# Performance work log

Hardware: AMD Instinct MI355X
Metric: run time of the kernel (lower is better)

Reference implementation:

```python
import jax, jax.numpy as jnp
import numpy as np

N_NODES = 4096
N_EDGES = 65536
BS = 16
LEAKY_SLOPE = 0.01
BN_EPS = 1e-5


def _init(key, shape, scale=0.02):
    return (jax.random.normal(key, shape, dtype=jnp.float32) * scale)


def setup_inputs() -> dict:
    key = jax.random.key(0)
    ks = jax.random.split(key, 20)
    x_in = jax.random.normal(ks[0], (N_NODES, 8500), dtype=jnp.float32)
    edge_index = jax.random.randint(ks[1], (2, N_EDGES), 0, N_NODES, dtype=jnp.int64)
    return {
        "x_in": x_in,
        "edge_index": edge_index,
        # SAGEConv params: Wl (neighbor lin, with bias), Wr (root lin, no bias)
        "W1l": _init(ks[2], (320, 8500)), "b1": jnp.zeros((320,), jnp.float32), "W1r": _init(ks[3], (320, 8500)),
        "W2l": _init(ks[4], (180, 320)),  "b2": jnp.zeros((180,), jnp.float32), "W2r": _init(ks[5], (180, 320)),
        "W3l": _init(ks[6], (90, 180)),   "b3": jnp.zeros((90,), jnp.float32),  "W3r": _init(ks[7], (90, 180)),
        "W4l": _init(ks[8], (50, 90)),    "b4": jnp.zeros((50,), jnp.float32),  "W4r": _init(ks[9], (50, 90)),
        "Wf1": _init(ks[10], (32, 50)),   "bf1": jnp.zeros((32,), jnp.float32),
        "Wf2": _init(ks[11], (16, 32)),   "bf2": jnp.zeros((16,), jnp.float32),
        "Wf3": _init(ks[12], (1, 16)),    "bf3": jnp.zeros((1,), jnp.float32),
    }


def _sage(x, src, dst, Wl, bl, Wr):
    # PyG SAGEConv: out = lin_l(mean_{j in N(i)} x_j) + lin_r(x_i)
    agg = jax.ops.segment_sum(x[src], dst, num_segments=N_NODES)          # [N, F]
    deg = jax.ops.segment_sum(jnp.ones_like(dst, dtype=x.dtype), dst, num_segments=N_NODES)
    mean = agg / jnp.maximum(deg, 1.0)[:, None]
    return mean @ Wl.T + bl + x @ Wr.T


def _leaky(x):
    return jnp.where(x >= 0, x, LEAKY_SLOPE * x)


def _bn(x):
    # F.batch_norm(x, None, None, training=True): per-feature, biased var, no affine
    m = jnp.mean(x, axis=0)
    v = jnp.mean((x - m) ** 2, axis=0)
    return (x - m) / jnp.sqrt(v + BN_EPS)


def reference(x_in, edge_index,
              W1l, b1, W1r, W2l, b2, W2r, W3l, b3, W3r, W4l, b4, W4r,
              Wf1, bf1, Wf2, bf2, Wf3, bf3):
    src, dst = edge_index[0], edge_index[1]
    x = _bn(_leaky(_sage(x_in, src, dst, W1l, b1, W1r)))
    x = _bn(_leaky(_sage(x, src, dst, W2l, b2, W2r)))
    x = _bn(_leaky(_sage(x, src, dst, W3l, b3, W3r)))
    x = _bn(_leaky(_sage(x, src, dst, W4l, b4, W4r)))
    # get_batch: label i -> floor(i / (N/BS)); global_add_pool == segment sum
    x = x.reshape(BS, N_NODES // BS, -1).sum(axis=1)                      # [BS, 50]
    x = x @ Wf1.T + bf1
    x = x @ Wf2.T + bf2
    x = x @ Wf3.T + bf3
    return x
```

## Files before the change

kernel.cpp:

```cpp
#include <hip/hip_runtime.h>
#include <stdint.h>

#define NN 4096
#define NE 65536
#define LEAKY 0.01f
#define BN_EPS 1e-5f

typedef float f32x4 __attribute__((ext_vector_type(4)));
typedef __bf16 bf16x8 __attribute__((ext_vector_type(8)));
typedef unsigned short u16x8 __attribute__((ext_vector_type(8)));

static __device__ __forceinline__ unsigned short f2bf(float v) {
  unsigned int u = __float_as_uint(v);
  u += 0x7fff + ((u >> 16) & 1);
  return (unsigned short)(u >> 16);
}

typedef __attribute__((address_space(1))) void gvoid;
typedef __attribute__((address_space(3))) void lvoid;

static __device__ __forceinline__ void async16(const void* g, void* l) {
  __builtin_amdgcn_global_load_lds((gvoid*)(uintptr_t)g,
                                   (lvoid*)(uint32_t)(uintptr_t)l, 16, 0, 0);
}


static __device__ __forceinline__ void pack_w_seg(int lblk, const float* __restrict__ Wl,
                                                  const float* __restrict__ Wr,
                                                  unsigned short* __restrict__ dst,
                                                  int Fout, int Fin, int Kp, int Np) {
  int nb = Kp >> 3;
  int idx = lblk * 256 + threadIdx.x;
  if (idx >= Np * nb) return;
  int row = idx / nb, kb = idx - row * nb;
  int g = kb >> 3, b = kb & 7;
  int dkb = (g << 3) | ((b + row) & 7);
  const float* src = nullptr;
  if (row < Fout)          src = Wl + (size_t)row * Fin;
  else if (row < 2 * Fout) src = Wr + (size_t)(row - Fout) * Fin;
  u16x8 st;
#pragma unroll
  for (int o = 0; o < 8; ++o) {
    int k = kb * 8 + o;
    float v = (src && k < Fin) ? src[k] : 0.f;
    st[o] = f2bf(v);
  }
  *(u16x8*)&dst[(size_t)row * Kp + dkb * 8] = st;
}

#define PX_BLK   17024
#define PW1_BLK   2660
#define PW2_BLK     60
#define PW3_BLK     24
#define PW4_BLK      8
#define CD_BLK     256
#define SETUP_BLK (PX_BLK + PW1_BLK + PW2_BLK + PW3_BLK + PW4_BLK + CD_BLK)

__global__ __launch_bounds__(256) void setup_all(
    const float* __restrict__ x, const int* __restrict__ dsti,
    const float* __restrict__ W1l, const float* __restrict__ W1r,
    const float* __restrict__ W2l, const float* __restrict__ W2r,
    const float* __restrict__ W3l, const float* __restrict__ W3r,
    const float* __restrict__ W4l, const float* __restrict__ W4r,
    unsigned short* __restrict__ xbf, unsigned short* __restrict__ wb1,
    unsigned short* __restrict__ wb2, unsigned short* __restrict__ wb3,
    unsigned short* __restrict__ wb4, int* __restrict__ deg) {
  int blk = blockIdx.x;
  if (blk < PX_BLK) {
    int idx = blk * 256 + threadIdx.x;
    int row = idx / 1064, kb = idx - row * 1064;
    int g = kb >> 3, b = kb & 7;
    int dkb = (g << 3) | ((b + row) & 7);
    const float* src = x + (size_t)row * 8500 + kb * 8;
    float v[8];
    if (kb < 1062) {
      f32x4 a = *(const f32x4*)src;
      f32x4 c = *(const f32x4*)(src + 4);
#pragma unroll
      for (int o = 0; o < 4; ++o) { v[o] = a[o]; v[o + 4] = c[o]; }
    } else {
#pragma unroll
      for (int o = 0; o < 8; ++o) {
        int k = kb * 8 + o;
        v[o] = (k < 8500) ? x[(size_t)row * 8500 + k] : 0.f;
      }
    }
    u16x8 st;
#pragma unroll
    for (int o = 0; o < 8; ++o) st[o] = f2bf(v[o]);
    *(u16x8*)&xbf[(size_t)row * 8512 + dkb * 8] = st;
  } else if (blk < PX_BLK + PW1_BLK) {
    pack_w_seg(blk - PX_BLK, W1l, W1r, wb1, 320, 8500, 8512, 640);
  } else if (blk < PX_BLK + PW1_BLK + PW2_BLK) {
    pack_w_seg(blk - PX_BLK - PW1_BLK, W2l, W2r, wb2, 180, 320, 320, 384);
  } else if (blk < PX_BLK + PW1_BLK + PW2_BLK + PW3_BLK) {
    pack_w_seg(blk - PX_BLK - PW1_BLK - PW2_BLK, W3l, W3r, wb3, 90, 180, 192, 256);
  } else if (blk < PX_BLK + PW1_BLK + PW2_BLK + PW3_BLK + PW4_BLK) {
    pack_w_seg(blk - PX_BLK - PW1_BLK - PW2_BLK - PW3_BLK, W4l, W4r, wb4, 50, 90, 128, 128);
  } else {
    int e = (blk - (SETUP_BLK - CD_BLK)) * 256 + threadIdx.x;
    atomicAdd(&deg[dsti[e]], 1);
  }
}


__global__ __launch_bounds__(1024) void scan_deg(const int* __restrict__ deg,
                                                 int* __restrict__ off) {
  __shared__ int s[NN];
  int t = threadIdx.x;
  for (int i = t; i < NN; i += 1024) s[i] = deg[i];
  __syncthreads();
  for (int step = 1; step < NN; step <<= 1) {
    int v[4];
#pragma unroll
    for (int j = 0; j < 4; ++j) {
      int i = t + j * 1024;
      v[j] = (i >= step) ? s[i - step] : 0;
    }
    __syncthreads();
#pragma unroll
    for (int j = 0; j < 4; ++j) s[t + j * 1024] += v[j];
    __syncthreads();
  }
  for (int i = t; i < NN; i += 1024) off[i] = (i == 0) ? 0 : s[i - 1];
}

__global__ void scatter_edges(const int* __restrict__ src_idx,
                              const int* __restrict__ dst_idx,
                              const int* __restrict__ off, int* __restrict__ cursor,
                              int* __restrict__ eix) {
  int e = blockIdx.x * 256 + threadIdx.x;
  if (e < NE) {
    int d = dst_idx[e];
    int pos = atomicAdd(&cursor[d], 1);
    eix[off[d] + pos] = src_idx[e];
  }
}

__global__ __launch_bounds__(256) void gemm_bt(const unsigned short* __restrict__ A,
                                               const unsigned short* __restrict__ B,
                                               float* __restrict__ C, int N, int K) {
  __shared__ unsigned short smem[2 * 128 * 64];
  unsigned short* As = smem;
  unsigned short* Bs = smem + 128 * 64;

  const int t = threadIdx.x;
  const int bm = blockIdx.x, bn = blockIdx.y;
  const int lane = t & 63;
  const int wave = t >> 6;
  const int wm = (wave & 1) * 64, wn = (wave >> 1) * 64;
  const int l16 = lane & 15, quad = lane >> 4;

  const int ksteps = K >> 6;
  const int gz = (int)gridDim.z;
  const int per = (ksteps + gz - 1) / gz;
  const int k0 = (int)blockIdx.z * per;
  int k1 = k0 + per; if (k1 > ksteps) k1 = ksteps;

  f32x4 zero = {0.f, 0.f, 0.f, 0.f};
  f32x4 acc[4][4];
#pragma unroll
  for (int i = 0; i < 4; ++i)
#pragma unroll
    for (int j = 0; j < 4; ++j) acc[i][j] = zero;

  const int srow = t >> 3;
  const int scol = (t & 7) * 8;
  const unsigned short* Abase = A + (size_t)(bm * 128) * K + scol;
  const unsigned short* Bbase = B + (size_t)(bn * 128) * K + scol;

  for (int kt = k0; kt < k1; ++kt) {
    const unsigned short* Ag = Abase + kt * 64;
    const unsigned short* Bg = Bbase + kt * 64;
#pragma unroll
    for (int p = 0; p < 4; ++p) {
      int row = p * 32 + srow;
      async16(Ag + (size_t)row * K, &As[row * 64 + scol]);
    }
#pragma unroll
    for (int p = 0; p < 4; ++p) {
      int row = p * 32 + srow;
      async16(Bg + (size_t)row * K, &Bs[row * 64 + scol]);
    }
    __syncthreads();
#pragma unroll
    for (int kh = 0; kh < 2; ++kh) {
      const int s8 = ((kh * 4 + quad + l16) & 7) * 8;
      bf16x8 af[4], bfr[4];
#pragma unroll
      for (int i = 0; i < 4; ++i)
        af[i] = *(const bf16x8*)&As[(wm + i * 16 + l16) * 64 + s8];
#pragma unroll
      for (int j = 0; j < 4; ++j)
        bfr[j] = *(const bf16x8*)&Bs[(wn + j * 16 + l16) * 64 + s8];
#pragma unroll
      for (int i = 0; i < 4; ++i)
#pragma unroll
        for (int j = 0; j < 4; ++j)
          acc[i][j] = __builtin_amdgcn_mfma_f32_16x16x32_bf16(af[i], bfr[j], acc[i][j], 0, 0, 0);
    }
    __syncthreads();
  }

  const bool use_atomic = (gridDim.z > 1);
#pragma unroll
  for (int i = 0; i < 4; ++i) {
    int rbase = bm * 128 + wm + i * 16 + quad * 4;
#pragma unroll
    for (int j = 0; j < 4; ++j) {
      int col = bn * 128 + wn + j * 16 + l16;
      float* cp = C + (size_t)rbase * N + col;
#pragma unroll
      for (int r = 0; r < 4; ++r) {
        if (use_atomic) atomicAdd(cp + (size_t)r * N, acc[i][j][r]);
        else            cp[(size_t)r * N] = acc[i][j][r];
      }
    }
  }
}

__global__ void sage_agg(const float* __restrict__ y, const int* __restrict__ off,
                         const int* __restrict__ deg, const int* __restrict__ eix,
                         const float* __restrict__ bias, float* __restrict__ z,
                         int F, int ldy) {
  int i = blockIdx.x;
  int f = blockIdx.y * 64 + threadIdx.x;
  if (f >= F) return;
  int start = off[i], d = deg[i];
  float s = 0.f;
  for (int e = 0; e < d; ++e) {
    int src = eix[start + e];
    s += y[(size_t)src * ldy + f];
  }
  int dm = d > 1 ? d : 1;
  float v = s / (float)dm + y[(size_t)i * ldy + F + f] + bias[f];
  z[(size_t)i * F + f] = (v >= 0.f) ? v : LEAKY * v;
}


__global__ __launch_bounds__(256) void bn_part(const float* __restrict__ z,
                                               float* __restrict__ sums, int F) {
  int tx = threadIdx.x, ty = threadIdx.y;
  int f = blockIdx.x * 64 + tx;
  float s = 0.f, s2 = 0.f;
  if (f < F) {
    int r0 = blockIdx.y * 512 + ty * 128;
    for (int j = 0; j < 128; ++j) {
      float v = z[(size_t)(r0 + j) * F + f];
      s += v; s2 += v * v;
    }
  }
  __shared__ float ls[4][64], ls2[4][64];
  ls[ty][tx] = s; ls2[ty][tx] = s2;
  __syncthreads();
  if (ty == 0 && f < F) {
    float S  = ls[0][tx] + ls[1][tx] + ls[2][tx] + ls[3][tx];
    float S2 = ls2[0][tx] + ls2[1][tx] + ls2[2][tx] + ls2[3][tx];
    atomicAdd(&sums[f], S);
    atomicAdd(&sums[F + f], S2);
  }
}

__global__ void bn_norm8(const float* __restrict__ z, const float* __restrict__ sums,
                         unsigned short* __restrict__ xout, int F, int Kp) {
  int nb = Kp >> 3;
  int idx = blockIdx.x * 256 + threadIdx.x;
  int row = idx / nb, kb = idx - row * nb;
  int g = kb >> 3, b = kb & 7;
  int dkb = (g << 3) | ((b + row) & 7);
  u16x8 st;
#pragma unroll
  for (int o = 0; o < 8; ++o) {
    int k = kb * 8 + o;
    float v = 0.f;
    if (k < F) {
      float m  = sums[k] * (1.f / NN);
      float var = sums[F + k] * (1.f / NN) - m * m;
      float rs = rsqrtf(var + BN_EPS);
      v = (z[(size_t)row * F + k] - m) * rs;
    }
    st[o] = f2bf(v);
  }
  *(u16x8*)&xout[(size_t)row * Kp + dkb * 8] = st;
}

__global__ void pool_fc(const float* __restrict__ z,
                        const float* __restrict__ sums,
                        const float* __restrict__ Wf1, const float* __restrict__ bf1,
                        const float* __restrict__ Wf2, const float* __restrict__ bf2,
                        const float* __restrict__ Wf3, const float* __restrict__ bf3,
                        float* __restrict__ out) {
  __shared__ float pool[50];
  __shared__ float h1[32], h2[16];
  int b = blockIdx.x, t = threadIdx.x;
  if (t < 50) {
    float s = 0.f;
    for (int r = 0; r < 256; ++r) s += z[(size_t)(b * 256 + r) * 50 + t];
    float m  = sums[t] * (1.f / NN);
    float var = sums[50 + t] * (1.f / NN) - m * m;
    float rs = rsqrtf(var + BN_EPS);
    pool[t] = (s - 256.f * m) * rs;
  }
  __syncthreads();
  if (t < 32) {
    float s = bf1[t];
    for (int f = 0; f < 50; ++f) s += pool[f] * Wf1[t * 50 + f];
    h1[t] = s;
  }
  __syncthreads();
  if (t < 16) {
    float s = bf2[t];
    for (int f = 0; f < 32; ++f) s += h1[f] * Wf2[t * 32 + f];
    h2[t] = s;
  }
  __syncthreads();
  if (t == 0) {
    float s = bf3[0];
    for (int f = 0; f < 16; ++f) s += h2[f] * Wf3[f];
    out[b] = s;
  }
}


extern "C" void kernel_launch(void* const* d_in, const int* in_sizes, int n_in,
                              void* d_out, int out_size, void* d_ws, size_t ws_size,
                              hipStream_t stream) {
  const float* x_in = (const float*)d_in[0];
  const int* ei = (const int*)d_in[1];
  const float* W1l = (const float*)d_in[2];
  const float* b1  = (const float*)d_in[3];
  const float* W1r = (const float*)d_in[4];
  const float* W2l = (const float*)d_in[5];
  const float* b2  = (const float*)d_in[6];
  const float* W2r = (const float*)d_in[7];
  const float* W3l = (const float*)d_in[8];
  const float* b3  = (const float*)d_in[9];
  const float* W3r = (const float*)d_in[10];
  const float* W4l = (const float*)d_in[11];
  const float* b4  = (const float*)d_in[12];
  const float* W4r = (const float*)d_in[13];
  const float* Wf1 = (const float*)d_in[14];
  const float* bf1 = (const float*)d_in[15];
  const float* Wf2 = (const float*)d_in[16];
  const float* bf2 = (const float*)d_in[17];
  const float* Wf3 = (const float*)d_in[18];
  const float* bf3 = (const float*)d_in[19];
  float* out = (float*)d_out;
  (void)in_sizes; (void)n_in; (void)out_size;

  char* ws = (char*)d_ws;
  size_t off = 0;
  auto alloc = [&](size_t bytes) -> void* {
    void* p = ws + off;
    off = (off + bytes + 255) & ~(size_t)255;
    return p;
  };
  unsigned short* xbf = (unsigned short*)alloc((size_t)NN * 8512 * 2);
  unsigned short* wb1 = (unsigned short*)alloc((size_t)640 * 8512 * 2);
  unsigned short* wb2 = (unsigned short*)alloc((size_t)384 * 320 * 2);
  unsigned short* wb3 = (unsigned short*)alloc((size_t)256 * 192 * 2);
  unsigned short* wb4 = (unsigned short*)alloc((size_t)128 * 128 * 2);
  float* y    = (float*)alloc((size_t)NN * 640 * 4);
  float* z    = (float*)alloc((size_t)NN * 320 * 4);
  int* deg    = (int*)alloc(NN * 4);
  int* cursor = (int*)alloc(NN * 4);
  float* bnsum = (float*)alloc(1280 * 4);
  int* offb   = (int*)alloc(NN * 4);
  int* eix    = (int*)alloc(NE * 4);
  if (ws_size < off) return;
  float* bns1 = bnsum;
  float* bns2 = bnsum + 640;
  float* bns3 = bnsum + 1000;
  float* bns4 = bnsum + 1180;

  hipMemsetAsync(deg, 0, 2 * NN * 4 + 1280 * 4, stream);
  hipMemsetAsync(y, 0, (size_t)NN * 640 * 4, stream);

  setup_all<<<dim3(SETUP_BLK), dim3(256), 0, stream>>>(
      x_in, ei + NE, W1l, W1r, W2l, W2r, W3l, W3r, W4l, W4r,
      xbf, wb1, wb2, wb3, wb4, deg);
  scan_deg<<<dim3(1), dim3(1024), 0, stream>>>(deg, offb);
  scatter_edges<<<dim3(NE / 256), dim3(256), 0, stream>>>(ei, ei + NE, offb, cursor, eix);

  gemm_bt<<<dim3(32, 5, 8), dim3(256), 0, stream>>>(xbf, wb1, y, 640, 8512);
  sage_agg<<<dim3(NN, 5), dim3(64), 0, stream>>>(y, offb, deg, eix, b1, z, 320, 640);
  bn_part<<<dim3(5, 8), dim3(64, 4), 0, stream>>>(z, bns1, 320);
  bn_norm8<<<dim3(NN * 40 / 256), dim3(256), 0, stream>>>(z, bns1, xbf, 320, 320);

  gemm_bt<<<dim3(32, 3, 1), dim3(256), 0, stream>>>(xbf, wb2, y, 384, 320);
  sage_agg<<<dim3(NN, 3), dim3(64), 0, stream>>>(y, offb, deg, eix, b2, z, 180, 384);
  bn_part<<<dim3(3, 8), dim3(64, 4), 0, stream>>>(z, bns2, 180);
  bn_norm8<<<dim3(NN * 24 / 256), dim3(256), 0, stream>>>(z, bns2, xbf, 180, 192);

  gemm_bt<<<dim3(32, 2, 1), dim3(256), 0, stream>>>(xbf, wb3, y, 256, 192);
  sage_agg<<<dim3(NN, 2), dim3(64), 0, stream>>>(y, offb, deg, eix, b3, z, 90, 256);
  bn_part<<<dim3(2, 8), dim3(64, 4), 0, stream>>>(z, bns3, 90);
  bn_norm8<<<dim3(NN * 16 / 256), dim3(256), 0, stream>>>(z, bns3, xbf, 90, 128);

  gemm_bt<<<dim3(32, 1, 1), dim3(256), 0, stream>>>(xbf, wb4, y, 128, 128);
  sage_agg<<<dim3(NN, 1), dim3(64), 0, stream>>>(y, offb, deg, eix, b4, z, 50, 128);
  bn_part<<<dim3(1, 8), dim3(64, 4), 0, stream>>>(z, bns4, 50);

  pool_fc<<<dim3(16), dim3(64), 0, stream>>>(z, bns4, Wf1, bf1, Wf2, bf2, Wf3, bf3, out);
}
```

Before: 559.5 us.

## Replace atomic split-K with partial buffers plus reduce, vectorize neighbor aggregation

The first-layer GEMM now writes four split-K partial results to separate slices of an enlarged buffer instead of atomically adding into a zeroed output. A new reduce4 kernel sums the slices, which also removes the memset of y. The sage_agg kernel is rewritten to use float4 loads and stage edge indices in shared memory. It splits each node's edges across four thread rows and reduces them through shared memory. The trade is an extra reduction pass and four times the workspace in exchange for removing atomic contention and improving gather bandwidth.

```diff
diff --git a/kernel.cpp b/kernel.cpp
--- a/kernel.cpp
+++ b/kernel.cpp
@@ -139,7 +139,8 @@
 
 __global__ __launch_bounds__(256) void gemm_bt(const unsigned short* __restrict__ A,
                                                const unsigned short* __restrict__ B,
-                                               float* __restrict__ C, int N, int K) {
+                                               float* __restrict__ C, int N, int K,
+                                               int M) {
   __shared__ unsigned short smem[2 * 128 * 64];
   unsigned short* As = smem;
   unsigned short* Bs = smem + 128 * 64;
@@ -202,39 +203,68 @@
     __syncthreads();
   }
 
-  const bool use_atomic = (gridDim.z > 1);
+  float* Cb = C + (size_t)blockIdx.z * M * N;
 #pragma unroll
   for (int i = 0; i < 4; ++i) {
     int rbase = bm * 128 + wm + i * 16 + quad * 4;
 #pragma unroll
     for (int j = 0; j < 4; ++j) {
       int col = bn * 128 + wn + j * 16 + l16;
-      float* cp = C + (size_t)rbase * N + col;
-#pragma unroll
-      for (int r = 0; r < 4; ++r) {
-        if (use_atomic) atomicAdd(cp + (size_t)r * N, acc[i][j][r]);
-        else            cp[(size_t)r * N] = acc[i][j][r];
-      }
-    }
-  }
-}
-
-__global__ void sage_agg(const float* __restrict__ y, const int* __restrict__ off,
-                         const int* __restrict__ deg, const int* __restrict__ eix,
-                         const float* __restrict__ bias, float* __restrict__ z,
-                         int F, int ldy) {
+      float* cp = Cb + (size_t)rbase * N + col;
+#pragma unroll
+      for (int r = 0; r < 4; ++r) cp[(size_t)r * N] = acc[i][j][r];
+    }
+  }
+}
+
+__global__ void reduce4(float* __restrict__ y) {
+  int idx = blockIdx.x * 256 + threadIdx.x;
+  f32x4* p = (f32x4*)y;
+  const int S = NN * 640 / 4;
+  f32x4 v = p[idx];
+  v += p[idx + S];
+  v += p[idx + 2 * S];
+  v += p[idx + 3 * S];
+  p[idx] = v;
+}
+
+__global__ __launch_bounds__(256) void sage_agg(
+    const float* __restrict__ y, const int* __restrict__ off,
+    const int* __restrict__ deg, const int* __restrict__ eix,
+    const float* __restrict__ bias, float* __restrict__ z, int F, int ldy) {
   int i = blockIdx.x;
-  int f = blockIdx.y * 64 + threadIdx.x;
-  if (f >= F) return;
+  int tx = threadIdx.x, ty = threadIdx.y;
+  int f4 = (blockIdx.y * 64 + tx) * 4;
+  __shared__ int se[64];
+  __shared__ float red[3][64][4];
   int start = off[i], d = deg[i];
-  float s = 0.f;
-  for (int e = 0; e < d; ++e) {
-    int src = eix[start + e];
-    s += y[(size_t)src * ldy + f];
-  }
-  int dm = d > 1 ? d : 1;
-  float v = s / (float)dm + y[(size_t)i * ldy + F + f] + bias[f];
-  z[(size_t)i * F + f] = (v >= 0.f) ? v : LEAKY * v;
+  bool active = (f4 < F);
+  f32x4 s = {0.f, 0.f, 0.f, 0.f};
+  for (int base = 0; base < d; base += 64) {
+    __syncthreads();
+    if (ty == 0 && base + tx < d) se[tx] = eix[start + base + tx];
+    __syncthreads();
+    int end = d - base; if (end > 64) end = 64;
+    if (active) {
+      for (int e = ty; e < end; e += 4)
+        s += *(const f32x4*)&y[(size_t)se[e] * ldy + f4];
+    }
+  }
+  if (ty > 0) *(f32x4*)red[ty - 1][tx] = s;
+  __syncthreads();
+  if (ty == 0 && active) {
+    s += *(const f32x4*)red[0][tx];
+    s += *(const f32x4*)red[1][tx];
+    s += *(const f32x4*)red[2][tx];
+    float inv = 1.f / (float)(d > 1 ? d : 1);
+    int cnt = F - f4; if (cnt > 4) cnt = 4;
+    const float* yr = &y[(size_t)i * ldy + F + f4];
+    float* zo = &z[(size_t)i * F + f4];
+    for (int j = 0; j < cnt; ++j) {
+      float w = s[j] * inv + yr[j] + bias[f4 + j];
+      zo[j] = (w >= 0.f) ? w : LEAKY * w;
+    }
+  }
 }
 
 
@@ -360,7 +390,7 @@
   unsigned short* wb2 = (unsigned short*)alloc((size_t)384 * 320 * 2);
   unsigned short* wb3 = (unsigned short*)alloc((size_t)256 * 192 * 2);
   unsigned short* wb4 = (unsigned short*)alloc((size_t)128 * 128 * 2);
-  float* y    = (float*)alloc((size_t)NN * 640 * 4);
+  float* y    = (float*)alloc((size_t)4 * NN * 640 * 4);
   float* z    = (float*)alloc((size_t)NN * 320 * 4);
   int* deg    = (int*)alloc(NN * 4);
   int* cursor = (int*)alloc(NN * 4);
@@ -374,7 +404,6 @@
   float* bns4 = bnsum + 1180;
 
   hipMemsetAsync(deg, 0, 2 * NN * 4 + 1280 * 4, stream);
-  hipMemsetAsync(y, 0, (size_t)NN * 640 * 4, stream);
 
   setup_all<<<dim3(SETUP_BLK), dim3(256), 0, stream>>>(
       x_in, ei + NE, W1l, W1r, W2l, W2r, W3l, W3r, W4l, W4r,
@@ -382,23 +411,24 @@
   scan_deg<<<dim3(1), dim3(1024), 0, stream>>>(deg, offb);
   scatter_edges<<<dim3(NE / 256), dim3(256), 0, stream>>>(ei, ei + NE, offb, cursor, eix);
 
-  gemm_bt<<<dim3(32, 5, 8), dim3(256), 0, stream>>>(xbf, wb1, y, 640, 8512);
-  sage_agg<<<dim3(NN, 5), dim3(64), 0, stream>>>(y, offb, deg, eix, b1, z, 320, 640);
+  gemm_bt<<<dim3(32, 5, 4), dim3(256), 0, stream>>>(xbf, wb1, y, 640, 8512, NN);
+  reduce4<<<dim3(NN * 640 / 4 / 256), dim3(256), 0, stream>>>(y);
+  sage_agg<<<dim3(NN, 2), dim3(64, 4), 0, stream>>>(y, offb, deg, eix, b1, z, 320, 640);
   bn_part<<<dim3(5, 8), dim3(64, 4), 0, stream>>>(z, bns1, 320);
   bn_norm8<<<dim3(NN * 40 / 256), dim3(256), 0, stream>>>(z, bns1, xbf, 320, 320);
 
-  gemm_bt<<<dim3(32, 3, 1), dim3(256), 0, stream>>>(xbf, wb2, y, 384, 320);
-  sage_agg<<<dim3(NN, 3), dim3(64), 0, stream>>>(y, offb, deg, eix, b2, z, 180, 384);
+  gemm_bt<<<dim3(32, 3, 1), dim3(256), 0, stream>>>(xbf, wb2, y, 384, 320, NN);
+  sage_agg<<<dim3(NN, 1), dim3(64, 4), 0, stream>>>(y, offb, deg, eix, b2, z, 180, 384);
   bn_part<<<dim3(3, 8), dim3(64, 4), 0, stream>>>(z, bns2, 180);
   bn_norm8<<<dim3(NN * 24 / 256), dim3(256), 0, stream>>>(z, bns2, xbf, 180, 192);
 
-  gemm_bt<<<dim3(32, 2, 1), dim3(256), 0, stream>>>(xbf, wb3, y, 256, 192);
-  sage_agg<<<dim3(NN, 2), dim3(64), 0, stream>>>(y, offb, deg, eix, b3, z, 90, 256);
+  gemm_bt<<<dim3(32, 2, 1), dim3(256), 0, stream>>>(xbf, wb3, y, 256, 192, NN);
+  sage_agg<<<dim3(NN, 1), dim3(64, 4), 0, stream>>>(y, offb, deg, eix, b3, z, 90, 256);
   bn_part<<<dim3(2, 8), dim3(64, 4), 0, stream>>>(z, bns3, 90);
   bn_norm8<<<dim3(NN * 16 / 256), dim3(256), 0, stream>>>(z, bns3, xbf, 90, 128);
 
-  gemm_bt<<<dim3(32, 1, 1), dim3(256), 0, stream>>>(xbf, wb4, y, 128, 128);
-  sage_agg<<<dim3(NN, 1), dim3(64), 0, stream>>>(y, offb, deg, eix, b4, z, 50, 128);
+  gemm_bt<<<dim3(32, 1, 1), dim3(256), 0, stream>>>(xbf, wb4, y, 128, 128, NN);
+  sage_agg<<<dim3(NN, 1), dim3(64, 4), 0, stream>>>(y, offb, deg, eix, b4, z, 50, 128);
   bn_part<<<dim3(1, 8), dim3(64, 4), 0, stream>>>(z, bns4, 50);
 
   pool_fc<<<dim3(16), dim3(64), 0, stream>>>(z, bns4, Wf1, bf1, Wf2, bf2, Wf3, bf3, out);
```

After: 516.4 us. 7.7% less time.
